# Performance work log

Hardware: AMD Instinct MI355X
Metric: run time of the kernel (lower is better)

## Reference

```python
import jax, jax.numpy as jnp
import numpy as np


def setup_inputs() -> dict:
    key = jax.random.key(0)
    k1, k2 = jax.random.split(key)
    n, B = 64, 256
    return {
        "out_matrix": jax.random.normal(k1, (n, n, B), dtype=jnp.float32),
        "label_matrix": jax.random.normal(k2, (n, n, B), dtype=jnp.float32),
        "margin": jnp.ones((), dtype=jnp.float32),
        "sample_num": 64,
    }


def reference(out_matrix, label_matrix, margin, sample_num):
    # out_matrix, label_matrix: [n, n, B]; sample_num == n (rows fully used).
    out = jnp.transpose(out_matrix, (2, 0, 1))   # [B, n, n]
    lab = jnp.transpose(label_matrix, (2, 0, 1))  # [B, n, n]
    # Per batch slice, per row r: pairwise diffs d[j,k] = out[r,j]-out[r,k]
    d = out[..., :, None] - out[..., None, :]     # [B, n, n, n]
    l = lab[..., :, None] - lab[..., None, :]     # [B, n, n, n]
    # Hinge: relu(margin - d*l), summed over everything (diagonal contributes margin,
    # matching the original which includes j==k terms).
    loss = jnp.sum(jax.nn.relu(margin - d * l))
    # flat_accuracy per batch slice: argmax over dim 1 of the [n,n] slice,
    # i.e. axis=2 of the [B,n,n] layout (torch argmax(preds,1) on squeezed slice).
    correction_num = jnp.sum(jnp.argmax(out, axis=2) == jnp.argmax(lab, axis=2))
    return loss, correction_num
```

## Files before the change

### kernel.cpp

```cpp
#include <hip/hip_runtime.h>
#include <math.h>


constexpr int N = 64;
constexpr int B = 256;
constexpr int BCHUNK = 64;
constexpr int NJG = 16;
constexpr int JI = 4;
constexpr int THREADS = BCHUNK * NJG;
constexpr int NBLK = N * (B / BCHUNK);

__global__ __launch_bounds__(THREADS)
void pm_hinge_partial(const float* __restrict__ outm,
                      const float* __restrict__ labm,
                      const float* __restrict__ margin,
                      float* __restrict__ ws)
{
    __shared__ float o_s[N * BCHUNK];
    __shared__ float l_s[N * BCHUNK];
    __shared__ float wsum[NJG];

    const int r   = blockIdx.x;
    const int b0  = blockIdx.y * BCHUNK;
    const int t   = threadIdx.x;
    const int blk = blockIdx.y * N + r;

    const float* src_o = outm + (size_t)r * (N * B) + b0;
    const float* src_l = labm + (size_t)r * (N * B) + b0;
#pragma unroll
    for (int f = t; f < (N * BCHUNK) / 4; f += THREADS) {
        const int j  = f >> 4;
        const int b4 = (f & 15) * 4;
        *(float4*)(&o_s[j * BCHUNK + b4]) = *(const float4*)(src_o + j * B + b4);
        *(float4*)(&l_s[j * BCHUNK + b4]) = *(const float4*)(src_l + j * B + b4);
    }
    __syncthreads();

    const float m  = margin[0];
    const int   b  = t & 63;
    const int   jg = t >> 6;

    float oj[JI], lj[JI];
#pragma unroll
    for (int i = 0; i < JI; ++i) {
        oj[i] = o_s[(jg + NJG * i) * BCHUNK + b];
        lj[i] = l_s[(jg + NJG * i) * BCHUNK + b];
    }

    float acc = 0.0f;

#define TERM(i) acc += fmaxf(fmaf(-(oj[i] - ok), lj[i] - lk, m), 0.0f)

#pragma unroll 4
    for (int k = jg + 1; k <= jg + 16; ++k) {
        const float ok = o_s[k * BCHUNK + b], lk = l_s[k * BCHUNK + b];
        TERM(0);
    }
#pragma unroll 4
    for (int k = jg + 17; k <= jg + 32; ++k) {
        const float ok = o_s[k * BCHUNK + b], lk = l_s[k * BCHUNK + b];
        TERM(0); TERM(1);
    }
#pragma unroll 4
    for (int k = jg + 33; k <= jg + 48; ++k) {
        const float ok = o_s[k * BCHUNK + b], lk = l_s[k * BCHUNK + b];
        TERM(0); TERM(1); TERM(2);
    }
#pragma unroll 2
    for (int k = jg + 49; k < N; ++k) {
        const float ok = o_s[k * BCHUNK + b], lk = l_s[k * BCHUNK + b];
        TERM(0); TERM(1); TERM(2); TERM(3);
    }
#undef TERM

    float cnt = 0.0f;
    if (t < 64) {
        const int bb = t;
        float bo = o_s[bb]; int io = 0;
        float bl = l_s[bb]; int il = 0;
#pragma unroll 4
        for (int j = 1; j < N; ++j) {
            const float vo = o_s[j * BCHUNK + bb];
            if (vo > bo) { bo = vo; io = j; }
            const float vl = l_s[j * BCHUNK + bb];
            if (vl > bl) { bl = vl; il = j; }
        }
        const unsigned long long mask = __ballot(io == il);
        cnt = (float)__popcll(mask);
    }

#pragma unroll
    for (int off = 32; off > 0; off >>= 1)
        acc += __shfl_down(acc, off, 64);
    if (b == 0) wsum[jg] = acc;
    __syncthreads();
    if (t == 0) {
        float s = 0.0f;
#pragma unroll
        for (int w = 0; w < NJG; ++w) s += wsum[w];
        ws[blk] = s;
        ws[NBLK + blk] = cnt;
    }
}

__global__ __launch_bounds__(64)
void pm_hinge_reduce(const float* __restrict__ ws,
                     const float* __restrict__ margin,
                     float* __restrict__ dout)
{
    const int t = threadIdx.x;
    float s = 0.0f, c = 0.0f;
#pragma unroll
    for (int i = 0; i < NBLK / 64; ++i) {
        s += ws[t + 64 * i];
        c += ws[NBLK + t + 64 * i];
    }
#pragma unroll
    for (int off = 32; off > 0; off >>= 1) {
        s += __shfl_down(s, off, 64);
        c += __shfl_down(c, off, 64);
    }
    if (t == 0) {
        const float m = margin[0];
        dout[0] = 2.0f * s + (float)(N * (size_t)N * B) * fmaxf(m, 0.0f);
        dout[1] = c;
    }
}

extern "C" void kernel_launch(void* const* d_in, const int* in_sizes, int n_in,
                              void* d_out, int out_size, void* d_ws, size_t ws_size,
                              hipStream_t stream) {
    const float* outm   = (const float*)d_in[0];
    const float* labm   = (const float*)d_in[1];
    const float* margin = (const float*)d_in[2];
    float* out = (float*)d_out;
    float* ws  = (float*)d_ws;

    pm_hinge_partial<<<dim3(N, B / BCHUNK), THREADS, 0, stream>>>(outm, labm, margin, ws);
    pm_hinge_reduce<<<1, 64, 0, stream>>>(ws, margin, out);
}
```

Baseline: 69.35 us.

## Interleave out/label in shared memory and raise per-thread j register blocking

Stores out and label values interleaved as float2 in LDS, so each k step needs one 64-bit LDS read instead of two 32-bit reads. Halves the number of j-groups per block (512 threads) and doubles the j values held in registers per thread (8), raising arithmetic per LDS load. Also splits the accumulator in two to shorten the add dependency chain. The trade-off is fewer threads per block, more register pressure, and a longer unrolled triangular loop.

```diff
diff --git a/kernel.cpp b/kernel.cpp
--- a/kernel.cpp
+++ b/kernel.cpp
@@ -5,8 +5,8 @@
 constexpr int N = 64;
 constexpr int B = 256;
 constexpr int BCHUNK = 64;
-constexpr int NJG = 16;
-constexpr int JI = 4;
+constexpr int NJG = 8;
+constexpr int JI = 8;
 constexpr int THREADS = BCHUNK * NJG;
 constexpr int NBLK = N * (B / BCHUNK);
 
@@ -16,8 +16,7 @@
                       const float* __restrict__ margin,
                       float* __restrict__ ws)
 {
-    __shared__ float o_s[N * BCHUNK];
-    __shared__ float l_s[N * BCHUNK];
+    __shared__ __align__(16) float2 s[N * BCHUNK];
     __shared__ float wsum[NJG];
 
     const int r   = blockIdx.x;
@@ -31,8 +30,11 @@
     for (int f = t; f < (N * BCHUNK) / 4; f += THREADS) {
         const int j  = f >> 4;
         const int b4 = (f & 15) * 4;
-        *(float4*)(&o_s[j * BCHUNK + b4]) = *(const float4*)(src_o + j * B + b4);
-        *(float4*)(&l_s[j * BCHUNK + b4]) = *(const float4*)(src_l + j * B + b4);
+        const float4 o4 = *(const float4*)(src_o + j * B + b4);
+        const float4 l4 = *(const float4*)(src_l + j * B + b4);
+        float4* dst = (float4*)(&s[j * BCHUNK + b4]);
+        dst[0] = make_float4(o4.x, l4.x, o4.y, l4.y);
+        dst[1] = make_float4(o4.z, l4.z, o4.w, l4.w);
     }
     __syncthreads();
 
@@ -43,47 +45,38 @@
     float oj[JI], lj[JI];
 #pragma unroll
     for (int i = 0; i < JI; ++i) {
-        oj[i] = o_s[(jg + NJG * i) * BCHUNK + b];
-        lj[i] = l_s[(jg + NJG * i) * BCHUNK + b];
+        const float2 v = s[(jg + NJG * i) * BCHUNK + b];
+        oj[i] = v.x; lj[i] = v.y;
     }
 
-    float acc = 0.0f;
-
-#define TERM(i) acc += fmaxf(fmaf(-(oj[i] - ok), lj[i] - lk, m), 0.0f)
-
+    float acc0 = 0.0f, acc1 = 0.0f;
+#pragma unroll
+    for (int mr = 0; mr < 8; ++mr) {
+        const int kbeg = jg + 8 * mr + 1;
+        const int kend = (mr == 7) ? N : (jg + 8 * mr + 9);
 #pragma unroll 4
-    for (int k = jg + 1; k <= jg + 16; ++k) {
-        const float ok = o_s[k * BCHUNK + b], lk = l_s[k * BCHUNK + b];
-        TERM(0);
+        for (int k = kbeg; k < kend; ++k) {
+            const float2 v = s[k * BCHUNK + b];
+            const float ok = v.x, lk = v.y;
+#pragma unroll
+            for (int i = 0; i <= mr; ++i) {
+                const float tv = fmaxf(fmaf(ok - oj[i], lj[i] - lk, m), 0.0f);
+                if (i & 1) acc1 += tv; else acc0 += tv;
+            }
+        }
     }
-#pragma unroll 4
-    for (int k = jg + 17; k <= jg + 32; ++k) {
-        const float ok = o_s[k * BCHUNK + b], lk = l_s[k * BCHUNK + b];
-        TERM(0); TERM(1);
-    }
-#pragma unroll 4
-    for (int k = jg + 33; k <= jg + 48; ++k) {
-        const float ok = o_s[k * BCHUNK + b], lk = l_s[k * BCHUNK + b];
-        TERM(0); TERM(1); TERM(2);
-    }
-#pragma unroll 2
-    for (int k = jg + 49; k < N; ++k) {
-        const float ok = o_s[k * BCHUNK + b], lk = l_s[k * BCHUNK + b];
-        TERM(0); TERM(1); TERM(2); TERM(3);
-    }
-#undef TERM
+    float acc = acc0 + acc1;
 
     float cnt = 0.0f;
     if (t < 64) {
-        const int bb = t;
-        float bo = o_s[bb]; int io = 0;
-        float bl = l_s[bb]; int il = 0;
+        const float2 v0 = s[t];
+        float bo = v0.x; int io = 0;
+        float bl = v0.y; int il = 0;
 #pragma unroll 4
         for (int j = 1; j < N; ++j) {
-            const float vo = o_s[j * BCHUNK + bb];
-            if (vo > bo) { bo = vo; io = j; }
-            const float vl = l_s[j * BCHUNK + bb];
-            if (vl > bl) { bl = vl; il = j; }
+            const float2 v = s[j * BCHUNK + t];
+            if (v.x > bo) { bo = v.x; io = j; }
+            if (v.y > bl) { bl = v.y; il = j; }
         }
         const unsigned long long mask = __ballot(io == il);
         cnt = (float)__popcll(mask);
@@ -95,10 +88,10 @@
     if (b == 0) wsum[jg] = acc;
     __syncthreads();
     if (t == 0) {
-        float s = 0.0f;
+        float ssum = 0.0f;
 #pragma unroll
-        for (int w = 0; w < NJG; ++w) s += wsum[w];
-        ws[blk] = s;
+        for (int w = 0; w < NJG; ++w) ssum += wsum[w];
+        ws[blk] = ssum;
         ws[NBLK + blk] = cnt;
     }
 }
```

Result: no change. 69.63 us (+0.4%).
